# Kernel tuning notes

Hardware: AMD Instinct MI355X
Metric: run time of the kernel (lower is better)

Reference implementation:

```python
import jax, jax.numpy as jnp
import numpy as np
from jax import lax

DN = ('NCHW', 'OIHW', 'NCHW')


def _conv(x, w, b):
    y = lax.conv_general_dilated(x, w, window_strides=(1, 1), padding='SAME',
                                 dimension_numbers=DN)
    return y + b[None, :, None, None]


def _features(x, w1, b1, w2, b2, w3, b3):
    # conv1 -> conv2 -> conv3, no nonlinearities (as in source)
    return _conv(_conv(_conv(x, w1, b1), w2, b2), w3, b3)


def setup_inputs() -> dict:
    key = jax.random.key(0)
    ks = jax.random.split(key, 8)
    B, H, W = 4, 64, 64
    x1 = jax.random.normal(ks[0], (B, 1, H, W), dtype=jnp.float32)
    x2 = jax.random.normal(ks[1], (B, 1, H, W), dtype=jnp.float32)
    # He-ish init so the 3-conv stack stays numerically tame
    w1 = jax.random.normal(ks[2], (32, 1, 3, 3), dtype=jnp.float32) / np.sqrt(1 * 9)
    b1 = jax.random.normal(ks[3], (32,), dtype=jnp.float32) * 0.01
    w2 = jax.random.normal(ks[4], (64, 32, 3, 3), dtype=jnp.float32) / np.sqrt(32 * 9)
    b2 = jax.random.normal(ks[5], (64,), dtype=jnp.float32) * 0.01
    w3 = jax.random.normal(ks[6], (256, 64, 3, 3), dtype=jnp.float32) / np.sqrt(64 * 9)
    b3 = jax.random.normal(ks[7], (256,), dtype=jnp.float32) * 0.01
    return {'x1': x1, 'x2': x2, 'w1': w1, 'b1': b1, 'w2': w2, 'b2': b2,
            'w3': w3, 'b3': b3}


def reference(x1, x2, w1, b1, w2, b2, w3, b3):
    f1 = _features(x1, w1, b1, w2, b2, w3, b3)  # (B, C, H, W), C=256
    f2 = _features(x2, w1, b1, w2, b2, w3, b3)  # (B, C, H, W)
    B, C, H, W = f1.shape
    N = H * W
    f1f = f1.reshape(B, C, N).transpose(0, 2, 1)  # (B, N, C) queries
    f2f = f2.reshape(B, C, N).transpose(0, 2, 1)  # (B, N, C) keys
    # all-pairs squared L2 distance via expansion: ||a||^2 - 2 a.b + ||b||^2
    a2 = jnp.sum(f1f * f1f, axis=-1, keepdims=True)          # (B, N, 1)
    b2v = jnp.sum(f2f * f2f, axis=-1)[:, None, :]             # (B, 1, N)
    cross = jnp.einsum('bic,bjc->bij', f1f, f2f)              # (B, N, N) GEMM
    dist = a2 - 2.0 * cross + b2v                             # (B, N, N)
    idx = jnp.argmin(dist, axis=-1)                           # (B, N)
    # gather nearest x2 feature for every x1 spatial location
    target = jnp.take_along_axis(f2f, idx[:, :, None], axis=1)  # (B, N, C)
    target = target.transpose(0, 2, 1).reshape(B, C, H, W)
    return jnp.concatenate([f1, target], axis=1)              # (B, 2C, H, W)
```

## Files before the change

### kernel.cpp

```cpp
#include <hip/hip_runtime.h>
#include <cstdint>

#define NPX 4096

using bf16x8 = __attribute__((ext_vector_type(8))) short;
using f32x4  = __attribute__((ext_vector_type(4))) float;

__device__ inline unsigned short f2bf_rne(float x) {
    unsigned u = __float_as_uint(x);
    unsigned r = (u + 0x7fffu + ((u >> 16) & 1u)) >> 16;
    return (unsigned short)r;
}
__device__ inline float bf2f(unsigned short h) {
    return __uint_as_float(((unsigned)h) << 16);
}

#define GLL(gp, lp) __builtin_amdgcn_global_load_lds( \
    (const __attribute__((address_space(1))) void*)(gp), \
    (__attribute__((address_space(3))) void*)(lp), 16, 0, 0)

__global__ __launch_bounds__(256) void conv1_k(
    const float* __restrict__ x1, const float* __restrict__ x2,
    const float* __restrict__ w,  const float* __restrict__ bias,
    float* __restrict__ y1)
{
    int gid = blockIdx.x * 256 + threadIdx.x;
    int px  = gid & 4095;
    int co  = (gid >> 12) & 31;
    int img = gid >> 17;
    const float* xin = (img < 4) ? (x1 + (size_t)img * NPX)
                                 : (x2 + (size_t)(img - 4) * NPX);
    int r = px >> 6, c = px & 63;
    float acc = bias[co];
#pragma unroll
    for (int dy = 0; dy < 3; ++dy) {
        int rr = r + dy - 1;
        if (rr < 0 || rr > 63) continue;
#pragma unroll
        for (int dx = 0; dx < 3; ++dx) {
            int cc = c + dx - 1;
            if (cc < 0 || cc > 63) continue;
            acc = fmaf(w[co * 9 + dy * 3 + dx], xin[rr * 64 + cc], acc);
        }
    }
    y1[(size_t)img * 32 * NPX + (size_t)co * NPX + px] = acc;
}

__global__ __launch_bounds__(256) void wtrans_k(
    const float* __restrict__ w, float* __restrict__ wT,
    int CI9, int CO, int total)
{
    int gid = blockIdx.x * 256 + threadIdx.x;
    if (gid >= total) return;
    int k = gid / CO, co = gid - k * CO;
    wT[gid] = w[(size_t)co * CI9 + k];
}

template <int CI>
__global__ __launch_bounds__(256) void convg_k(
    const float* __restrict__ in,
    const float* __restrict__ wT,
    const float* __restrict__ bias,
    float* __restrict__ outA, float* __restrict__ outB,
    int strideA, int strideB, int COT)
{
    constexpr int CIC = 16;
    __shared__ __align__(16) float in_lds[CIC * 6 * 64];
    __shared__ __align__(16) float w_lds[CIC * 9 * 64];

    const int r0  = blockIdx.x * 4;
    const int img = blockIdx.y;
    const int cob = blockIdx.z * 64;
    const int tid = threadIdx.x;
    const int co4 = (tid & 15) * 4;
    const int pxg = tid >> 4;
    const int row_l = pxg >> 2;
    const int c0 = (pxg & 3) * 16;

    const float* ib = in + (size_t)img * CI * NPX;

    float acc[4][16];
#pragma unroll
    for (int e = 0; e < 4; ++e) {
        float bv = bias[cob + co4 + e];
#pragma unroll
        for (int p = 0; p < 16; ++p) acc[e][p] = bv;
    }

    for (int cic = 0; cic < CI; cic += CIC) {
        __syncthreads();
#pragma unroll
        for (int t = 0; t < 6; ++t) {
            int f = tid + t * 256;
            int ci = f / 96, rem = f - ci * 96;
            int dyr = rem >> 4, c4 = rem & 15;
            int gr = r0 + dyr - 1;
            float4 v = make_float4(0.f, 0.f, 0.f, 0.f);
            if (gr >= 0 && gr < 64)
                v = *(const float4*)&ib[(size_t)(cic + ci) * NPX + gr * 64 + c4 * 4];
            *(float4*)&in_lds[(ci * 6 + dyr) * 64 + c4 * 4] = v;
        }
#pragma unroll
        for (int t = 0; t < 9; ++t) {
            int f = tid + t * 256;
            int k = f >> 4, c4 = f & 15;
            *(float4*)&w_lds[k * 64 + c4 * 4] =
                *(const float4*)&wT[(size_t)(cic * 9 + k) * COT + cob + c4 * 4];
        }
        __syncthreads();

        for (int ci = 0; ci < CIC; ++ci) {
#pragma unroll
            for (int dy = 0; dy < 3; ++dy) {
                const float* rp = &in_lds[(ci * 6 + row_l + dy) * 64 + c0];
                float v[18];
                float left  = rp[(c0 == 0)  ? 0 : -1];
                float right = rp[(c0 == 48) ? 0 : 16];
                v[0]  = (c0 == 0)  ? 0.f : left;
                *(float4*)&v[1]  = *(const float4*)&rp[0];
                *(float4*)&v[5]  = *(const float4*)&rp[4];
                *(float4*)&v[9]  = *(const float4*)&rp[8];
                *(float4*)&v[13] = *(const float4*)&rp[12];
                v[17] = (c0 == 48) ? 0.f : right;
                const float* wp = &w_lds[(ci * 9 + dy * 3) * 64 + co4];
                float wv[3][4];
                *(float4*)&wv[0][0] = *(const float4*)&wp[0];
                *(float4*)&wv[1][0] = *(const float4*)&wp[64];
                *(float4*)&wv[2][0] = *(const float4*)&wp[128];
#pragma unroll
                for (int dx = 0; dx < 3; ++dx)
#pragma unroll
                    for (int e = 0; e < 4; ++e)
#pragma unroll
                        for (int p = 0; p < 16; ++p)
                            acc[e][p] = fmaf(wv[dx][e], v[p + dx], acc[e][p]);
            }
        }
    }

    float* dst = (img < 4) ? (outA + (size_t)img * strideA)
                           : (outB + (size_t)(img - 4) * strideB);
    dst += (size_t)(cob + co4) * NPX + (r0 + row_l) * 64 + c0;
#pragma unroll
    for (int e = 0; e < 4; ++e)
#pragma unroll
        for (int q = 0; q < 4; ++q)
            *(float4*)&dst[(size_t)e * NPX + q * 4] = *(float4*)&acc[e][q * 4];
}

__global__ __launch_bounds__(256) void wprep_k(
    const float* __restrict__ w3, unsigned short* __restrict__ w3f)
{
    int i = blockIdx.x * 256 + threadIdx.x;
    if (i >= 147456) return;
    int tap = i % 9;  int t2 = i / 9;
    int ci = t2 & 63; int co = t2 >> 6;
    float v = w3[(size_t)(co * 64 + ci) * 9 + tap];
    unsigned short hi = f2bf_rne(v);
    unsigned short lo = f2bf_rne(v - bf2f(hi));
    int cg = co >> 7, wm = (co >> 6) & 1, mf = (co >> 4) & 3, l15 = co & 15;
    int ch = ci >> 5, q = (ci >> 3) & 3, e = ci & 7;
    int lane = q * 16 + l15;
    size_t o = (size_t)(cg * 2 + wm) * 73728 + tap * 8192 + ch * 4096
             + mf * 512 + lane * 8 + e;
    w3f[o] = hi;
    w3f[o + 2048] = lo;
}

__global__ __launch_bounds__(256) void y2prep_k(
    const float* __restrict__ y2,
    unsigned short* __restrict__ h, unsigned short* __restrict__ l)
{
    const int rg = blockIdx.x;
    const int img = blockIdx.y;
    const int tid = threadIdx.x;
    const size_t base = ((size_t)img * 66 + rg) * 4096;
    if (rg == 0 || rg == 65) {
#pragma unroll
        for (int t = 0; t < 16; ++t) {
            h[base + tid + t * 256] = 0;
            l[base + tid + t * 256] = 0;
        }
        return;
    }
    __shared__ float T[64][65];
    const int row = rg - 1;
#pragma unroll
    for (int t = 0; t < 16; ++t) {
        int ii = tid + t * 256;
        int ci = ii >> 6, col = ii & 63;
        T[ci][col] = y2[(size_t)img * 262144 + (size_t)ci * NPX + row * 64 + col];
    }
    __syncthreads();
#pragma unroll
    for (int t = 0; t < 16; ++t) {
        int ii = tid + t * 256;
        int ci = ii & 63, px = ii >> 6;
        float v = T[ci][px];
        unsigned short hi = f2bf_rne(v);
        h[base + px * 64 + ci] = hi;
        l[base + px * 64 + ci] = f2bf_rne(v - bf2f(hi));
    }
}

__global__ __launch_bounds__(512, 2) void conv3m_k(
    const unsigned short* __restrict__ y2ph,
    const unsigned short* __restrict__ y2pl,
    const unsigned short* __restrict__ w3f,
    const float* __restrict__ b3,
    float* __restrict__ out, float* __restrict__ f2)
{
    __shared__ unsigned short xlds[49152];
    const int pxg = blockIdx.x;
    const int img = blockIdx.y;
    const int cg  = blockIdx.z;
    const int tid = threadIdx.x;
    const int lane = tid & 63;
    const int wid = tid >> 6;
    const int wm = wid >> 2, wn = wid & 3;
    const int q16 = lane >> 4, l15 = lane & 15;
    const int r0 = pxg * 4;
    const int px0 = pxg * 256;
    const int cob = cg * 128;

    const unsigned short* yh = y2ph + (size_t)img * 270336;
    const unsigned short* yl = y2pl + (size_t)img * 270336;
#pragma unroll
    for (int it = 0; it < 12; ++it) {
        int dbase = it * 8192 + wid * 1024;
        int d = dbase + lane * 16;
        int s = d >= 49152;
        int r = d - (s ? 49152 : 0);
        int pxl = r >> 7;
        int kbs = (r >> 4) & 7;
        int kb  = kbs ^ (pxl & 7);
        int rg  = r0 + (pxl >> 6);
        int col = pxl & 63;
        const unsigned short* src = (s ? yl : yh) + ((rg << 6) + col) * 64 + kb * 8;
        GLL(src, (char*)xlds + dbase);
    }

    const unsigned short* wbase = w3f + (size_t)(cg * 2 + wm) * 73728 + lane * 8;
    bf16x8 awh[2][4], awl[2][4];
#pragma unroll
    for (int mf = 0; mf < 4; ++mf) {
        awh[0][mf] = *(const bf16x8*)(wbase + mf * 512);
        awl[0][mf] = *(const bf16x8*)(wbase + 2048 + mf * 512);
    }

    f32x4 acc[4][4];
#pragma unroll
    for (int mf = 0; mf < 4; ++mf) {
        float bv[4];
#pragma unroll
        for (int r = 0; r < 4; ++r)
            bv[r] = b3[cob + wm * 64 + mf * 16 + q16 * 4 + r];
#pragma unroll
        for (int nf = 0; nf < 4; ++nf)
#pragma unroll
            for (int r = 0; r < 4; ++r) acc[mf][nf][r] = bv[r];
    }

    const int plb = wn * 64 + 64 + l15;
    const int key_m = (lane + 7) & 7;
    const int key_0 = lane & 7;
    const int key_p = (lane + 1) & 7;
    const bf16x8 z8 = {0, 0, 0, 0, 0, 0, 0, 0};

    __syncthreads();

#pragma unroll
    for (int ch = 0; ch < 2; ++ch) {
#pragma unroll
        for (int tap = 0; tap < 9; ++tap) {
            const int st = ch * 9 + tap;
            const int cur = st & 1;
            if (st < 17) {
                const int nst = st + 1;
                const int nch = nst / 9, ntap = nst % 9;
#pragma unroll
                for (int mf = 0; mf < 4; ++mf) {
                    awh[cur ^ 1][mf] = *(const bf16x8*)(wbase + ntap * 8192 + nch * 4096 + mf * 512);
                    awl[cur ^ 1][mf] = *(const bf16x8*)(wbase + ntap * 8192 + nch * 4096 + 2048 + mf * 512);
                }
            }
            const int dy = tap / 3 - 1, dx = tap % 3 - 1;
            const int key = (dx < 0) ? key_m : ((dx > 0) ? key_p : key_0);
            bf16x8 bh[4], bl[4];
#pragma unroll
            for (int nf = 0; nf < 4; ++nf) {
                int row = plb + nf * 16 + dy * 64 + dx;
                row = row < 0 ? 0 : (row > 383 ? 383 : row);
                int kbs = (q16 + ch * 4) ^ key;
                int ba = row * 128 + kbs * 16;
                bh[nf] = *(const bf16x8*)((const char*)xlds + ba);
                bl[nf] = *(const bf16x8*)((const char*)xlds + ba + 49152);
                if (dx < 0 && nf == 0) {
                    bh[nf] = (l15 == 0) ? z8 : bh[nf];
                    bl[nf] = (l15 == 0) ? z8 : bl[nf];
                }
                if (dx > 0 && nf == 3) {
                    bh[nf] = (l15 == 15) ? z8 : bh[nf];
                    bl[nf] = (l15 == 15) ? z8 : bl[nf];
                }
            }
#pragma unroll
            for (int mf = 0; mf < 4; ++mf)
#pragma unroll
                for (int nf = 0; nf < 4; ++nf) {
                    f32x4 c = acc[mf][nf];
                    c = __builtin_amdgcn_mfma_f32_16x16x32_bf16(awh[cur][mf], bh[nf], c, 0, 0, 0);
                    c = __builtin_amdgcn_mfma_f32_16x16x32_bf16(awh[cur][mf], bl[nf], c, 0, 0, 0);
                    c = __builtin_amdgcn_mfma_f32_16x16x32_bf16(awl[cur][mf], bh[nf], c, 0, 0, 0);
                    acc[mf][nf] = c;
                }
        }
    }

    float* dst = (img < 4) ? out + (size_t)img * 512 * NPX
                           : f2  + (size_t)(img - 4) * 256 * NPX;
#pragma unroll
    for (int mf = 0; mf < 4; ++mf)
#pragma unroll
        for (int nf = 0; nf < 4; ++nf)
#pragma unroll
            for (int r = 0; r < 4; ++r) {
                int co = cob + wm * 64 + mf * 16 + q16 * 4 + r;
                int px = px0 + wn * 64 + nf * 16 + l15;
                dst[(size_t)co * NPX + px] = acc[mf][nf][r];
            }
}

__global__ __launch_bounds__(256) void splitT_k(
    const float* __restrict__ src, size_t srcStride,
    unsigned short* __restrict__ dh, unsigned short* __restrict__ dl)
{
    __shared__ float T[64][65];
    const int m0 = blockIdx.x * 64, k0 = blockIdx.y * 64, b = blockIdx.z;
    const float* s = src + (size_t)b * srcStride;
    const int tid = threadIdx.x;
    const int cm = tid & 63, rk = tid >> 6;
#pragma unroll
    for (int t = 0; t < 16; ++t)
        T[rk + t * 4][cm] = s[(size_t)(k0 + rk + t * 4) * NPX + m0 + cm];
    __syncthreads();
    const int ck = tid & 63, rm = tid >> 6;
#pragma unroll
    for (int t = 0; t < 16; ++t) {
        int m = rm + t * 4;
        float v = T[ck][m];
        unsigned short hi = f2bf_rne(v);
        float lo = v - bf2f(hi);
        size_t o = ((size_t)b * NPX + m0 + m) * 256 + k0 + ck;
        dh[o] = hi;
        dl[o] = f2bf_rne(lo);
    }
}

__global__ __launch_bounds__(256) void normb_k(
    const float* __restrict__ f2, float* __restrict__ normB,
    unsigned long long* __restrict__ minkey)
{
    int gid = blockIdx.x * 256 + threadIdx.x;
    int b = gid >> 12, j = gid & 4095;
    const float* p = f2 + (size_t)b * 256 * NPX + j;
    float s = 0.f;
#pragma unroll 8
    for (int c = 0; c < 256; ++c) {
        float v = p[(size_t)c * NPX];
        s = fmaf(v, v, s);
    }
    normB[gid] = s;
    minkey[gid] = ~0ull;
}

__global__ __launch_bounds__(256) void gemm_argmin_mfma_k(
    const unsigned short* __restrict__ f1h, const unsigned short* __restrict__ f1l,
    const unsigned short* __restrict__ f2h, const unsigned short* __restrict__ f2l,
    const float* __restrict__ normB,
    unsigned long long* __restrict__ minkey)
{
    __shared__ unsigned short lds[4][4096];
    const int b  = blockIdx.z;
    const int i0 = blockIdx.y * 128;
    const int j0 = blockIdx.x * 128;
    const int tid  = threadIdx.x;
    const int lane = tid & 63;
    const int w    = tid >> 6;
    const int wm   = w >> 1, wn = w & 1;

    const int srow  = w * 32 + (lane >> 2);
    const int skoff = (lane & 3) * 8;
    const unsigned short* pAh = f1h + ((size_t)b * NPX + i0 + srow) * 256 + skoff;
    const unsigned short* pAl = f1l + ((size_t)b * NPX + i0 + srow) * 256 + skoff;
    const unsigned short* pBh = f2h + ((size_t)b * NPX + j0 + srow) * 256 + skoff;
    const unsigned short* pBl = f2l + ((size_t)b * NPX + j0 + srow) * 256 + skoff;
    unsigned short* l0 = &lds[0][0] + w * 1024;
    unsigned short* l1 = &lds[1][0] + w * 1024;
    unsigned short* l2 = &lds[2][0] + w * 1024;
    unsigned short* l3 = &lds[3][0] + w * 1024;

    const int aoff = (wm * 64 + (lane & 15)) * 32 + (lane >> 4) * 8;
    const int boff = (wn * 64 + (lane & 15)) * 32 + (lane >> 4) * 8;

    const f32x4 zero = {0.f, 0.f, 0.f, 0.f};
    f32x4 acc[4][4];
#pragma unroll
    for (int i = 0; i < 4; ++i)
#pragma unroll
        for (int j = 0; j < 4; ++j) acc[i][j] = zero;

    for (int kb = 0; kb < 256; kb += 32) {
        __syncthreads();
        GLL(pAh,            l0);
        GLL(pAh + 16 * 256, l0 + 512);
        GLL(pAl,            l1);
        GLL(pAl + 16 * 256, l1 + 512);
        GLL(pBh,            l2);
        GLL(pBh + 16 * 256, l2 + 512);
        GLL(pBl,            l3);
        GLL(pBl + 16 * 256, l3 + 512);
        pAh += 32; pAl += 32; pBh += 32; pBl += 32;
        __syncthreads();

        bf16x8 ah[4], al[4], bh[4], bl[4];
#pragma unroll
        for (int mf = 0; mf < 4; ++mf) {
            ah[mf] = *(const bf16x8*)&lds[0][aoff + mf * 512];
            al[mf] = *(const bf16x8*)&lds[1][aoff + mf * 512];
        }
#pragma unroll
        for (int nf = 0; nf < 4; ++nf) {
            bh[nf] = *(const bf16x8*)&lds[2][boff + nf * 512];
            bl[nf] = *(const bf16x8*)&lds[3][boff + nf * 512];
        }
#pragma unroll
        for (int mf = 0; mf < 4; ++mf)
#pragma unroll
            for (int nf = 0; nf < 4; ++nf) {
                f32x4 c = acc[mf][nf];
                c = __builtin_amdgcn_mfma_f32_16x16x32_bf16(ah[mf], bh[nf], c, 0, 0, 0);
                c = __builtin_amdgcn_mfma_f32_16x16x32_bf16(ah[mf], bl[nf], c, 0, 0, 0);
                c = __builtin_amdgcn_mfma_f32_16x16x32_bf16(al[mf], bh[nf], c, 0, 0, 0);
                c = __builtin_amdgcn_mfma_f32_16x16x32_bf16(al[mf], bl[nf], c, 0, 0, 0);
                acc[mf][nf] = c;
            }
    }

    float nbv[4];
    const float* nbp = normB + b * 4096 + j0 + wn * 64 + (lane & 15);
#pragma unroll
    for (int nf = 0; nf < 4; ++nf) nbv[nf] = nbp[nf * 16];
    const int jcol = j0 + wn * 64 + (lane & 15);

#pragma unroll
    for (int mf = 0; mf < 4; ++mf) {
#pragma unroll
        for (int reg = 0; reg < 4; ++reg) {
            unsigned long long kmin = ~0ull;
#pragma unroll
            for (int nf = 0; nf < 4; ++nf) {
                float d = fmaf(-2.f, acc[mf][nf][reg], nbv[nf]);
                unsigned u = __float_as_uint(d);
                u = (u & 0x80000000u) ? ~u : (u | 0x80000000u);
                unsigned long long key =
                    ((unsigned long long)u << 32) | (unsigned)(jcol + nf * 16);
                kmin = kmin < key ? kmin : key;
            }
#pragma unroll
            for (int s = 1; s < 16; s <<= 1) {
                unsigned long long o = __shfl_xor(kmin, s, 64);
                kmin = kmin < o ? kmin : o;
            }
            if ((lane & 15) == 0) {
                int i = i0 + wm * 64 + mf * 16 + (lane >> 4) * 4 + reg;
                atomicMin(&minkey[(size_t)b * 4096 + i], kmin);
            }
        }
    }
}

__global__ __launch_bounds__(256) void gather_k(
    const unsigned long long* __restrict__ minkey,
    const float* __restrict__ f2, float* __restrict__ out)
{
    int b  = blockIdx.y;
    int px = blockIdx.x * 256 + threadIdx.x;
    int idx = (int)(unsigned)(minkey[(size_t)b * 4096 + px] & 0xffffffffu);
    const float* src = f2 + (size_t)b * 256 * NPX;
    float* dst = out + (size_t)b * 512 * NPX + (size_t)256 * NPX + px;
#pragma unroll 4
    for (int c = 0; c < 256; ++c)
        dst[(size_t)c * NPX] = src[(size_t)c * NPX + idx];
}

extern "C" void kernel_launch(void* const* d_in, const int* in_sizes, int n_in,
                              void* d_out, int out_size, void* d_ws, size_t ws_size,
                              hipStream_t stream)
{
    const float* x1 = (const float*)d_in[0];
    const float* x2 = (const float*)d_in[1];
    const float* w1 = (const float*)d_in[2];
    const float* b1 = (const float*)d_in[3];
    const float* w2 = (const float*)d_in[4];
    const float* b2 = (const float*)d_in[5];
    const float* w3 = (const float*)d_in[6];
    const float* b3 = (const float*)d_in[7];
    float* out = (float*)d_out;
    char* ws = (char*)d_ws;

    float* y1 = (float*)(ws);
    float* y2 = (float*)(ws + 4194304);
    float* f2 = (float*)(ws + 12582912);
    float* normB = (float*)(ws + 29360128);
    unsigned long long* minkey = (unsigned long long*)(ws + 29425664);
    float* w2T = (float*)(ws + 29556736);
    unsigned short* w3f  = (unsigned short*)(ws + 29630464);
    unsigned short* y2ph = (unsigned short*)(ws + 30220288);
    unsigned short* y2pl = (unsigned short*)(ws + 34545664);
    unsigned short* f1h  = (unsigned short*)(ws);
    unsigned short* f1l  = (unsigned short*)(ws + 30220288);
    unsigned short* f2h  = (unsigned short*)(ws + 38871040);
    unsigned short* f2l  = (unsigned short*)(ws + 47259648);

    wtrans_k<<<72, 256, 0, stream>>>(w2, w2T, 32 * 9, 64, 64 * 288);
    wprep_k<<<576, 256, 0, stream>>>(w3, w3f);

    conv1_k<<<4096, 256, 0, stream>>>(x1, x2, w1, b1, y1);

    convg_k<32><<<dim3(16, 8, 1), 256, 0, stream>>>(
        y1, w2T, b2, y2, y2 + (size_t)4 * 64 * NPX, 64 * NPX, 64 * NPX, 64);

    y2prep_k<<<dim3(66, 8), 256, 0, stream>>>(y2, y2ph, y2pl);

    conv3m_k<<<dim3(16, 8, 2), 512, 0, stream>>>(y2ph, y2pl, w3f, b3, out, f2);

    normb_k<<<64, 256, 0, stream>>>(f2, normB, minkey);

    splitT_k<<<dim3(64, 4, 4), 256, 0, stream>>>(out, (size_t)512 * NPX, f1h, f1l);
    splitT_k<<<dim3(64, 4, 4), 256, 0, stream>>>(f2,  (size_t)256 * NPX, f2h, f2l);

    gemm_argmin_mfma_k<<<dim3(32, 32, 4), 256, 0, stream>>>(
        f1h, f1l, f2h, f2l, normB, minkey);

    gather_k<<<dim3(16, 4), 256, 0, stream>>>(minkey, f2, out);
}
```

Before: 373.7 us.

## Double-buffer LDS tiles, swizzle layout, and drop low*low MFMA term

After: 377.9 us. No clear change (+1.1%).

```diff
diff --git a/kernel.cpp b/kernel.cpp
--- a/kernel.cpp
+++ b/kernel.cpp
@@ -380,7 +380,7 @@
     const float* __restrict__ normB,
     unsigned long long* __restrict__ minkey)
 {
-    __shared__ unsigned short lds[4][4096];
+    __shared__ unsigned short lds[2][4][4096];
     const int b  = blockIdx.z;
     const int i0 = blockIdx.y * 128;
     const int j0 = blockIdx.x * 128;
@@ -390,18 +390,28 @@
     const int wm   = w >> 1, wn = w & 1;
 
     const int srow  = w * 32 + (lane >> 2);
-    const int skoff = (lane & 3) * 8;
+    const int skoff = (((lane & 3) ^ ((lane >> 3) & 3))) * 8;
     const unsigned short* pAh = f1h + ((size_t)b * NPX + i0 + srow) * 256 + skoff;
     const unsigned short* pAl = f1l + ((size_t)b * NPX + i0 + srow) * 256 + skoff;
     const unsigned short* pBh = f2h + ((size_t)b * NPX + j0 + srow) * 256 + skoff;
     const unsigned short* pBl = f2l + ((size_t)b * NPX + j0 + srow) * 256 + skoff;
-    unsigned short* l0 = &lds[0][0] + w * 1024;
-    unsigned short* l1 = &lds[1][0] + w * 1024;
-    unsigned short* l2 = &lds[2][0] + w * 1024;
-    unsigned short* l3 = &lds[3][0] + w * 1024;
-
-    const int aoff = (wm * 64 + (lane & 15)) * 32 + (lane >> 4) * 8;
-    const int boff = (wn * 64 + (lane & 15)) * 32 + (lane >> 4) * 8;
+    const unsigned short* pAh2 = pAh + 16 * 256;
+    const unsigned short* pAl2 = pAl + 16 * 256;
+    const unsigned short* pBh2 = pBh + 16 * 256;
+    const unsigned short* pBl2 = pBl + 16 * 256;
+
+#define STAGE(p) do { \
+        GLL(pAh,  &lds[p][0][0] + w * 1024); GLL(pAh2, &lds[p][0][0] + w * 1024 + 512); \
+        GLL(pAl,  &lds[p][1][0] + w * 1024); GLL(pAl2, &lds[p][1][0] + w * 1024 + 512); \
+        GLL(pBh,  &lds[p][2][0] + w * 1024); GLL(pBh2, &lds[p][2][0] + w * 1024 + 512); \
+        GLL(pBl,  &lds[p][3][0] + w * 1024); GLL(pBl2, &lds[p][3][0] + w * 1024 + 512); \
+        pAh += 32; pAl += 32; pBh += 32; pBl += 32; \
+        pAh2 += 32; pAl2 += 32; pBh2 += 32; pBl2 += 32; } while (0)
+
+    const int r15 = lane & 15;
+    const int swz = (r15 >> 1) & 3;
+    const int aoff = (wm * 64 + r15) * 32 + (((lane >> 4) ^ swz)) * 8;
+    const int boff = (wn * 64 + r15) * 32 + (((lane >> 4) ^ swz)) * 8;
 
     const f32x4 zero = {0.f, 0.f, 0.f, 0.f};
     f32x4 acc[4][4];
@@ -410,29 +420,24 @@
 #pragma unroll
         for (int j = 0; j < 4; ++j) acc[i][j] = zero;
 
-    for (int kb = 0; kb < 256; kb += 32) {
-        __syncthreads();
-        GLL(pAh,            l0);
-        GLL(pAh + 16 * 256, l0 + 512);
-        GLL(pAl,            l1);
-        GLL(pAl + 16 * 256, l1 + 512);
-        GLL(pBh,            l2);
-        GLL(pBh + 16 * 256, l2 + 512);
-        GLL(pBl,            l3);
-        GLL(pBl + 16 * 256, l3 + 512);
-        pAh += 32; pAl += 32; pBh += 32; pBl += 32;
-        __syncthreads();
+    STAGE(0);
+    __syncthreads();
+
+#pragma unroll
+    for (int kb = 0; kb < 8; ++kb) {
+        const int cur = kb & 1;
+        if (kb < 7) STAGE(cur ^ 1);
 
         bf16x8 ah[4], al[4], bh[4], bl[4];
 #pragma unroll
         for (int mf = 0; mf < 4; ++mf) {
-            ah[mf] = *(const bf16x8*)&lds[0][aoff + mf * 512];
-            al[mf] = *(const bf16x8*)&lds[1][aoff + mf * 512];
+            ah[mf] = *(const bf16x8*)&lds[cur][0][aoff + mf * 512];
+            al[mf] = *(const bf16x8*)&lds[cur][1][aoff + mf * 512];
         }
 #pragma unroll
         for (int nf = 0; nf < 4; ++nf) {
-            bh[nf] = *(const bf16x8*)&lds[2][boff + nf * 512];
-            bl[nf] = *(const bf16x8*)&lds[3][boff + nf * 512];
+            bh[nf] = *(const bf16x8*)&lds[cur][2][boff + nf * 512];
+            bl[nf] = *(const bf16x8*)&lds[cur][3][boff + nf * 512];
         }
 #pragma unroll
         for (int mf = 0; mf < 4; ++mf)
@@ -442,16 +447,17 @@
                 c = __builtin_amdgcn_mfma_f32_16x16x32_bf16(ah[mf], bh[nf], c, 0, 0, 0);
                 c = __builtin_amdgcn_mfma_f32_16x16x32_bf16(ah[mf], bl[nf], c, 0, 0, 0);
                 c = __builtin_amdgcn_mfma_f32_16x16x32_bf16(al[mf], bh[nf], c, 0, 0, 0);
-                c = __builtin_amdgcn_mfma_f32_16x16x32_bf16(al[mf], bl[nf], c, 0, 0, 0);
                 acc[mf][nf] = c;
             }
-    }
+        __syncthreads();
+    }
+#undef STAGE
 
     float nbv[4];
-    const float* nbp = normB + b * 4096 + j0 + wn * 64 + (lane & 15);
+    const float* nbp = normB + b * 4096 + j0 + wn * 64 + r15;
 #pragma unroll
     for (int nf = 0; nf < 4; ++nf) nbv[nf] = nbp[nf * 16];
-    const int jcol = j0 + wn * 64 + (lane & 15);
+    const int jcol = j0 + wn * 64 + r15;
 
 #pragma unroll
     for (int mf = 0; mf < 4; ++mf) {
@@ -472,7 +478,7 @@
                 unsigned long long o = __shfl_xor(kmin, s, 64);
                 kmin = kmin < o ? kmin : o;
             }
-            if ((lane & 15) == 0) {
+            if (r15 == 0) {
                 int i = i0 + wm * 64 + mf * 16 + (lane >> 4) * 4 + reg;
                 atomicMin(&minkey[(size_t)b * 4096 + i], kmin);
             }
```
